# Kernel tuning notes

Hardware: AMD Instinct MI355X
Metric: run time of the kernel (lower is better)

Reference implementation:

```python
import jax, jax.numpy as jnp
import numpy as np

S = 1024      # seq_len
H = 768       # hidden_size
L = 50        # num_labels
E = 65536     # num_edges
SW = 10       # span_width


def setup_inputs() -> dict:
    key = jax.random.key(0)
    ks = jax.random.split(key, 10)
    hidden_states = jax.random.normal(ks[0], (1, S, H), jnp.float32)
    src = jax.random.randint(ks[1], (E,), 0, S)
    tgt = jax.random.randint(ks[2], (E,), 0, S)
    lbl = jax.random.randint(ks[3], (E,), 0, L)
    edges = jnp.stack([src, tgt, lbl], axis=-1)[None].astype(jnp.int32)  # [1,E,3]
    gcn_W = (jax.random.normal(ks[4], (L, H, H)) * 0.02).astype(jnp.float32)
    gcn_b = jnp.zeros((L, H), jnp.float32)
    attn_w = (jax.random.normal(ks[5], (H,)) * 0.02).astype(jnp.float32)
    attn_b = jnp.zeros((), jnp.float32)
    D = 3 * H
    ms_W1 = (jax.random.normal(ks[6], (D, D)) * 0.02).astype(jnp.float32)
    ms_b1 = jnp.zeros((D,), jnp.float32)
    ms_W2 = (jax.random.normal(ks[7], (D,)) * 0.02).astype(jnp.float32)
    ms_b2 = jnp.zeros((), jnp.float32)
    ant_W = (jax.random.normal(ks[8], (2 * D,)) * 0.02).astype(jnp.float32)
    ant_b = jnp.zeros((), jnp.float32)
    # candidate spans exactly as generate_candidate_spans with span_width=SW
    starts, ends = [], []
    for i in range(S):
        for j in range(i + 1, min(i + SW, S)):
            starts.append(i)
            ends.append(j)
    span_starts = jnp.asarray(np.array(starts, dtype=np.int32))
    span_ends = jnp.asarray(np.array(ends, dtype=np.int32))
    topk = int(S * 0.4)  # seq_lens*0.4 with all-ones attention mask
    return {
        'hidden_states': hidden_states, 'edges': edges,
        'gcn_W': gcn_W, 'gcn_b': gcn_b,
        'attn_w': attn_w, 'attn_b': attn_b,
        'ms_W1': ms_W1, 'ms_b1': ms_b1, 'ms_W2': ms_W2, 'ms_b2': ms_b2,
        'ant_W': ant_W, 'ant_b': ant_b,
        'span_starts': span_starts, 'span_ends': span_ends, 'topk': topk,
    }


def reference(hidden_states, edges, gcn_W, gcn_b, attn_w, attn_b,
              ms_W1, ms_b1, ms_W2, ms_b2, ant_W, ant_b,
              span_starts, span_ends, topk):
    B, Sq, Hd = hidden_states.shape  # B == 1
    nl = gcn_W.shape[0]
    x = hidden_states[0]  # [S,H]

    # ---- GCNLayer: per-label linear + scatter-add + degree norm + relu ----
    src = edges[0, :, 0]
    tgt = edges[0, :, 1]
    lbl = edges[0, :, 2]
    # aggregate source embeddings by (target,label): equivalent to applying
    # W_l per edge then index_add, since the transform is linear per label.
    seg = tgt * nl + lbl                               # [E]
    src_emb = x[src]                                   # [E,H]  gather
    agg = jax.ops.segment_sum(src_emb, seg, num_segments=Sq * nl)
    agg = agg.reshape(Sq, nl, Hd)                      # [S,L,H]
    cnt = jax.ops.segment_sum(jnp.ones_like(seg, jnp.float32), seg,
                              num_segments=Sq * nl).reshape(Sq, nl)
    out = jnp.einsum('slh,lhd->sd', agg, gcn_W) + cnt @ gcn_b  # [S,H]
    degree = jnp.clip(cnt.sum(axis=1), 1.0)[:, None]
    gcn_out = jax.nn.relu(out / degree)

    # combine_strategy == 'add'
    emb = x + gcn_out                                  # [S,H]

    # ---- SpanRepresentation: attention pooling over each span ----
    offs = jnp.arange(SW)                              # span length <= SW
    pos = span_starts[:, None] + offs                  # [N,SW]
    valid = pos <= span_ends[:, None]
    pos_c = jnp.minimum(pos, Sq - 1)
    win = emb[pos_c]                                   # [N,SW,H] gather
    scores = win @ attn_w + attn_b                     # [N,SW]
    scores = jnp.where(valid, scores, -1e9)
    aw = jax.nn.softmax(scores, axis=1)
    attn_out = jnp.einsum('nw,nwh->nh', aw, win)       # [N,H]
    span_vec = jnp.concatenate([emb[span_starts], emb[span_ends], attn_out],
                               axis=-1)                # [N,3H]

    # ---- MentionScorer ----
    hdn = jax.nn.relu(span_vec @ ms_W1 + ms_b1)
    mention_scores = hdn @ ms_W2 + ms_b2               # [N]

    # ---- prune_spans: top-k ----
    topk_scores, topk_idx = jax.lax.top_k(mention_scores, topk)
    pruned = span_vec[topk_idx]                        # [k,3H]

    # ---- antecedent scores: linear over concat pair == sum of two matvecs ----
    D = span_vec.shape[-1]
    s_i = pruned @ ant_W[:D]                           # [k]
    s_j = pruned @ ant_W[D:]                           # [k]
    ant_scores = s_i[:, None] + s_j[None, :] + ant_b   # [k,k]
    # triu mask (antecedent must strictly precede the mention)
    k = pruned.shape[0]
    triu = jnp.triu(jnp.ones((k, k), bool), k=0)
    ant_scores = jnp.where(triu, -1e4, ant_scores)
    dummy = jnp.zeros((k, 1), ant_scores.dtype)
    ant_scores_with_dummy = jnp.concatenate([dummy, ant_scores], axis=1)  # [k,k+1]
    return ant_scores_with_dummy
```

## Files before the change

kernel.cpp:

```cpp
#include <hip/hip_runtime.h>
#include <stdint.h>

typedef __attribute__((ext_vector_type(4))) float f32x4;
typedef __attribute__((ext_vector_type(4))) int i32x4;
typedef __attribute__((ext_vector_type(8))) int i32x8;

#define S_TOK 1024
#define H_DIM 768
#define NLBL  50
#define NEDGE 65536
#define NSEG  (S_TOK * NLBL)
#define NSPAN 9171
#define MPAD  9216
#define DDIM  2304
#define KTOP  409

__device__ __forceinline__ unsigned short f32_to_bf16u(float f) {
  unsigned u = __float_as_uint(f);
  u += 0x7fffu + ((u >> 16) & 1u);
  return (unsigned short)(u >> 16);
}
__device__ __forceinline__ float bf16u_to_f32(unsigned short h) {
  return __uint_as_float(((unsigned)h) << 16);
}
__device__ __forceinline__ unsigned short pack_fp8x2(float a, float b) {
  return (unsigned short)(__builtin_amdgcn_cvt_pk_fp8_f32(a, b, 0, false) & 0xffff);
}
__device__ __forceinline__ unsigned pack_fp8x4(float a, float b, float c, float d) {
  int v = __builtin_amdgcn_cvt_pk_fp8_f32(a, b, 0, false);
  v = __builtin_amdgcn_cvt_pk_fp8_f32(c, d, v, true);
  return (unsigned)v;
}
__device__ __forceinline__ unsigned char pack_fp8x1(float a) {
  return (unsigned char)(__builtin_amdgcn_cvt_pk_fp8_f32(a, a, 0, false) & 0xff);
}

__device__ __forceinline__ void gl_lds16(const void* g, void* l) {
  __builtin_amdgcn_global_load_lds((const __attribute__((address_space(1))) void*)g,
                                   (__attribute__((address_space(3))) void*)l, 16, 0, 0);
}

__global__ __launch_bounds__(256) void convert_fp8(
    const float* __restrict__ in, unsigned* __restrict__ out, int nquads) {
  int i = blockIdx.x * 256 + threadIdx.x;
  if (i >= nquads) return;
  float4 v = ((const float4*)in)[i];
  out[i] = pack_fp8x4(v.x, v.y, v.z, v.w);
}

__global__ __launch_bounds__(256) void transpose_fp8_b(
    const float* __restrict__ in, unsigned char* __restrict__ out, int R, int C) {
  __shared__ float tile[32][33];
  size_t boff = (size_t)blockIdx.z * R * C;
  int tx = threadIdx.x & 31, ty = threadIdx.x >> 5;
  int c0 = blockIdx.x * 32, r0 = blockIdx.y * 32;
#pragma unroll
  for (int i = 0; i < 4; i++)
    tile[ty + 8 * i][tx] = in[boff + (size_t)(r0 + ty + 8 * i) * C + c0 + tx];
  __syncthreads();
#pragma unroll
  for (int i = 0; i < 4; i++)
    out[boff + (size_t)(c0 + ty + 8 * i) * R + r0 + tx] = pack_fp8x1(tile[tx][ty + 8 * i]);
}

__global__ void edge_count2(const int* __restrict__ edges, int* __restrict__ seg_count,
                            int* __restrict__ tgt_count) {
  int e = blockIdx.x * 256 + threadIdx.x;
  if (e >= NEDGE) return;
  int tgt = edges[e * 3 + 1], lbl = edges[e * 3 + 2];
  atomicAdd(&seg_count[tgt * NLBL + lbl], 1);
  atomicAdd(&tgt_count[tgt], 1);
}

__global__ __launch_bounds__(1024) void scan_t(
    const int* __restrict__ cnt, int* __restrict__ offs) {
  __shared__ int part[1024];
  int t = threadIdx.x;
  int c = cnt[t];
  part[t] = c;
  __syncthreads();
  for (int o = 1; o < 1024; o <<= 1) {
    int v = part[t];
    int u = (t >= o) ? part[t - o] : 0;
    __syncthreads();
    part[t] = v + u;
    __syncthreads();
  }
  offs[t] = part[t] - c;
  if (t == 1023) offs[1024] = part[t];
}

__global__ void edge_scatter_t(const int* __restrict__ edges, const int* __restrict__ tgt_off,
                               int* __restrict__ cursor, int* __restrict__ sorted_row) {
  int e = blockIdx.x * 256 + threadIdx.x;
  if (e >= NEDGE) return;
  int src = edges[e * 3], tgt = edges[e * 3 + 1], lbl = edges[e * 3 + 2];
  int pos = tgt_off[tgt] + atomicAdd(&cursor[tgt], 1);
  sorted_row[pos] = lbl * S_TOK + src;
}

template <int EPI>
__global__ __launch_bounds__(256) void gemm_fp8(
    const unsigned char* __restrict__ A, const unsigned char* __restrict__ B,
    unsigned char* __restrict__ Y, float* __restrict__ C,
    const float* __restrict__ b1, const float* __restrict__ w2,
    int M, int Nn, int Kb, int mb, size_t strideB, size_t strideY) {
  __shared__ unsigned char As[128 * 128];
  __shared__ unsigned char Bs[128 * 128];
  int im = blockIdx.x % mb, in_ = blockIdx.x / mb;
  int m0 = im * 128, n0 = in_ * 128;
  const unsigned char* Bl = B + (size_t)blockIdx.y * strideB;

  int t = threadIdx.x;
  int wave = t >> 6, lane = t & 63;
  int wr = wave >> 1, wc = wave & 1;
  int quad = lane >> 4, l15 = lane & 15;
  int lrow = lane >> 3;
  int lk = ((lane & 7) ^ lrow) << 4;

  f32x4 acc[4][4];
  f32x4 zero = {0.f, 0.f, 0.f, 0.f};
#pragma unroll
  for (int mi = 0; mi < 4; mi++)
#pragma unroll
    for (int ni = 0; ni < 4; ni++) acc[mi][ni] = zero;

  for (int kt = 0; kt < Kb; kt += 128) {
#pragma unroll
    for (int i = 0; i < 4; i++) {
      int c = i * 4 + wave;
      int r = c * 8 + lrow;
      gl_lds16(A + (size_t)(m0 + r) * Kb + kt + lk, &As[c * 1024]);
      gl_lds16(Bl + (size_t)(n0 + r) * Kb + kt + lk, &Bs[c * 1024]);
    }
    __syncthreads();
    i32x8 af[4], bg[4];
#pragma unroll
    for (int mi = 0; mi < 4; mi++) {
      int r = wr * 64 + mi * 16 + l15;
      int base = r * 128;
      i32x4 lo = *(const i32x4*)&As[base + (((2 * quad) ^ (r & 7)) << 4)];
      i32x4 hi = *(const i32x4*)&As[base + (((2 * quad + 1) ^ (r & 7)) << 4)];
      af[mi] = __builtin_shufflevector(lo, hi, 0, 1, 2, 3, 4, 5, 6, 7);
    }
#pragma unroll
    for (int ni = 0; ni < 4; ni++) {
      int r = wc * 64 + ni * 16 + l15;
      int base = r * 128;
      i32x4 lo = *(const i32x4*)&Bs[base + (((2 * quad) ^ (r & 7)) << 4)];
      i32x4 hi = *(const i32x4*)&Bs[base + (((2 * quad + 1) ^ (r & 7)) << 4)];
      bg[ni] = __builtin_shufflevector(lo, hi, 0, 1, 2, 3, 4, 5, 6, 7);
    }
#pragma unroll
    for (int mi = 0; mi < 4; mi++)
#pragma unroll
      for (int ni = 0; ni < 4; ni++)
        acc[mi][ni] = __builtin_amdgcn_mfma_scale_f32_16x16x128_f8f6f4(
            af[mi], bg[ni], acc[mi][ni], 0, 0, 0, 0x7f7f7f7f, 0, 0x7f7f7f7f);
    __syncthreads();
  }

  if (EPI == 0) {
    unsigned char* Yl = Y + (size_t)blockIdx.y * strideY;
#pragma unroll
    for (int mi = 0; mi < 4; mi++)
#pragma unroll
      for (int ni = 0; ni < 4; ni++)
#pragma unroll
        for (int r = 0; r < 4; r++)
          As[(wr * 64 + mi * 16 + quad * 4 + r) * 128 + wc * 64 + ni * 16 + l15] =
              pack_fp8x1(acc[mi][ni][r]);
    __syncthreads();
#pragma unroll
    for (int i = 0; i < 4; i++) {
      int idx = t + i * 256;
      int row = idx >> 3, off2 = (idx & 7) << 4;
      *(i32x4*)(Yl + (size_t)(m0 + row) * Nn + n0 + off2) = *(const i32x4*)&As[row * 128 + off2];
    }
  } else {
    float b1v[4], w2v[4];
#pragma unroll
    for (int ni = 0; ni < 4; ni++) {
      int gn = n0 + wc * 64 + ni * 16 + l15;
      b1v[ni] = b1[gn];
      w2v[ni] = w2[gn];
    }
#pragma unroll
    for (int mi = 0; mi < 4; mi++) {
      int gm = m0 + wr * 64 + mi * 16 + quad * 4;
      float part[4] = {0.f, 0.f, 0.f, 0.f};
#pragma unroll
      for (int ni = 0; ni < 4; ni++)
#pragma unroll
        for (int r = 0; r < 4; r++)
          part[r] += fmaxf(acc[mi][ni][r] + b1v[ni], 0.f) * w2v[ni];
#pragma unroll
      for (int o = 1; o < 16; o <<= 1)
#pragma unroll
        for (int r = 0; r < 4; r++) part[r] += __shfl_xor(part[r], o, 64);
      if (l15 == 0) {
#pragma unroll
        for (int r = 0; r < 4; r++)
          if (gm + r < M) atomicAdd(&C[gm + r], part[r]);
      }
    }
  }
}

__global__ __launch_bounds__(192) void gather_emb_kernel(
    const float* __restrict__ x, const unsigned char* __restrict__ Y,
    const int* __restrict__ tgt_off, const int* __restrict__ sorted_row,
    const int* __restrict__ seg_count, const float* __restrict__ gcn_b,
    float* __restrict__ emb) {
  int s = blockIdx.x;
  int t = threadIdx.x;
  int b = tgt_off[s], e = tgt_off[s + 1];
  float a0 = 0.f, a1 = 0.f, a2 = 0.f, a3 = 0.f;
  int p = b;
  for (; p + 1 < e; p += 2) {
    const unsigned* r0 = (const unsigned*)(Y + (size_t)sorted_row[p] * H_DIM);
    const unsigned* r1 = (const unsigned*)(Y + (size_t)sorted_row[p + 1] * H_DIM);
    unsigned w0 = r0[t], w1 = r1[t];
    a0 += __builtin_amdgcn_cvt_f32_fp8(w0, 0) + __builtin_amdgcn_cvt_f32_fp8(w1, 0);
    a1 += __builtin_amdgcn_cvt_f32_fp8(w0, 1) + __builtin_amdgcn_cvt_f32_fp8(w1, 1);
    a2 += __builtin_amdgcn_cvt_f32_fp8(w0, 2) + __builtin_amdgcn_cvt_f32_fp8(w1, 2);
    a3 += __builtin_amdgcn_cvt_f32_fp8(w0, 3) + __builtin_amdgcn_cvt_f32_fp8(w1, 3);
  }
  if (p < e) {
    unsigned w0 = ((const unsigned*)(Y + (size_t)sorted_row[p] * H_DIM))[t];
    a0 += __builtin_amdgcn_cvt_f32_fp8(w0, 0);
    a1 += __builtin_amdgcn_cvt_f32_fp8(w0, 1);
    a2 += __builtin_amdgcn_cvt_f32_fp8(w0, 2);
    a3 += __builtin_amdgcn_cvt_f32_fp8(w0, 3);
  }
  float deg = 0.f, b0 = 0.f, b1 = 0.f, b2 = 0.f, b3 = 0.f;
#pragma unroll 5
  for (int l = 0; l < NLBL; l++) {
    float c = (float)seg_count[s * NLBL + l];
    deg += c;
    float4 g = ((const float4*)(gcn_b + l * H_DIM))[t];
    b0 += c * g.x; b1 += c * g.y; b2 += c * g.z; b3 += c * g.w;
  }
  float dinv = 1.f / fmaxf(deg, 1.f);
  float4 xe = ((const float4*)(x + (size_t)s * H_DIM))[t];
  float4 o;
  o.x = xe.x + fmaxf((a0 + b0) * dinv, 0.f);
  o.y = xe.y + fmaxf((a1 + b1) * dinv, 0.f);
  o.z = xe.z + fmaxf((a2 + b2) * dinv, 0.f);
  o.w = xe.w + fmaxf((a3 + b3) * dinv, 0.f);
  ((float4*)(emb + (size_t)s * H_DIM))[t] = o;
}

__global__ __launch_bounds__(256) void span_kernel(
    const float* __restrict__ emb, const float* __restrict__ attn_w,
    unsigned char* __restrict__ spanv) {
  int i = blockIdx.x;
  int nsp = 1023 - i; if (nsp > 9) nsp = 9;
  if (nsp <= 0) return;
  int nrow = nsp + 1;
  __shared__ float rows[10][768];
  __shared__ float dsh[10];
  int t = threadIdx.x;
  for (int idx = t; idx < nrow * 384; idx += 256) {
    int r = idx / 384, c2 = idx % 384;
    float2 v = ((const float2*)(emb + (size_t)(i + r) * H_DIM))[c2];
    rows[r][c2 * 2] = v.x; rows[r][c2 * 2 + 1] = v.y;
  }
  __syncthreads();
  int wave = t >> 6, lane = t & 63;
  for (int w = wave; w < nrow; w += 4) {
    float p = 0.f;
#pragma unroll
    for (int q = 0; q < 12; q++) p += rows[w][lane + 64 * q] * attn_w[lane + 64 * q];
#pragma unroll
    for (int o = 1; o < 64; o <<= 1) p += __shfl_xor(p, o, 64);
    if (lane == 0) dsh[w] = p;
  }
  __syncthreads();
  float d[10], ex[10];
  float mx = -1e30f;
  for (int w = 0; w < nrow; w++) { d[w] = dsh[w]; mx = fmaxf(mx, d[w]); }
  for (int w = 0; w < nrow; w++) ex[w] = __expf(d[w] - mx);
  bool has2 = (t < 128);
  float n00 = ex[0] * rows[0][2 * t], n01 = ex[0] * rows[0][2 * t + 1];
  float n10 = 0.f, n11 = 0.f;
  if (has2) { n10 = ex[0] * rows[0][2 * t + 512]; n11 = ex[0] * rows[0][2 * t + 513]; }
  float S = ex[0];
  int dd = i - 1014;
  int base = 9 * i - (dd > 0 ? dd * (dd - 1) / 2 : 0);
  unsigned short s0a = pack_fp8x2(rows[0][2 * t], rows[0][2 * t + 1]);
  unsigned short s0b = has2 ? pack_fp8x2(rows[0][2 * t + 512], rows[0][2 * t + 513]) : (unsigned short)0;
  for (int k = 1; k <= nsp; k++) {
    S += ex[k];
    n00 += ex[k] * rows[k][2 * t]; n01 += ex[k] * rows[k][2 * t + 1];
    if (has2) { n10 += ex[k] * rows[k][2 * t + 512]; n11 += ex[k] * rows[k][2 * t + 513]; }
    float inv = 1.f / S;
    unsigned short* out16 = (unsigned short*)(spanv + (size_t)(base + k - 1) * DDIM);
    out16[t] = s0a;
    out16[384 + t] = pack_fp8x2(rows[k][2 * t], rows[k][2 * t + 1]);
    out16[768 + t] = pack_fp8x2(n00 * inv, n01 * inv);
    if (has2) {
      out16[t + 256] = s0b;
      out16[384 + t + 256] = pack_fp8x2(rows[k][2 * t + 512], rows[k][2 * t + 513]);
      out16[768 + t + 256] = pack_fp8x2(n10 * inv, n11 * inv);
    }
  }
}

__device__ __forceinline__ unsigned score_key(float s) {
  unsigned b = __float_as_uint(s);
  return (b & 0x80000000u) ? ~b : (b | 0x80000000u);
}

__global__ __launch_bounds__(1024) void topk_kernel(
    const float* __restrict__ scores, int* __restrict__ topk_idx) {
  __shared__ unsigned skeys[NSPAN];
  __shared__ int hist[16 * 256];
  __shared__ int hsum[256];
  __shared__ unsigned sh_prefix;
  __shared__ int sh_remaining, sh_cnt;
  __shared__ unsigned long long keys[512];
  int t = threadIdx.x;
  int wv = t >> 6;
  for (int i = t; i < NSPAN; i += 1024) skeys[i] = score_key(scores[i]);
  unsigned prefix = 0;
  int remaining = KTOP;
  for (int p = 3; p >= 0; p--) {
    for (int b = t; b < 16 * 256; b += 1024) hist[b] = 0;
    __syncthreads();
    for (int i = t; i < NSPAN; i += 1024) {
      unsigned u = skeys[i];
      bool ok = (p == 3) ? true : ((u >> ((p + 1) * 8)) == prefix);
      if (ok) atomicAdd(&hist[wv * 256 + ((u >> (p * 8)) & 0xff)], 1);
    }
    __syncthreads();
    if (t < 256) {
      int s = 0;
#pragma unroll
      for (int w = 0; w < 16; w++) s += hist[w * 256 + t];
      hsum[t] = s;
    }
    __syncthreads();
    if (t == 0) {
      int rem = remaining;
      int b = 255;
      for (;; b--) {
        int c = hsum[b];
        if (c >= rem) break;
        rem -= c;
      }
      sh_prefix = (prefix << 8) | (unsigned)b;
      sh_remaining = rem;
    }
    __syncthreads();
    prefix = sh_prefix;
    remaining = sh_remaining;
    __syncthreads();
  }
  unsigned kth = prefix;
  if (t == 0) sh_cnt = 0;
  __syncthreads();
  for (int i = t; i < NSPAN; i += 1024) {
    unsigned u = skeys[i];
    if (u >= kth) {
      int pos = atomicAdd(&sh_cnt, 1);
      if (pos < 512) keys[pos] = (((unsigned long long)(~u)) << 32) | (unsigned)i;
    }
  }
  __syncthreads();
  int cnt = sh_cnt < 512 ? sh_cnt : 512;
  for (int i = t; i < 512; i += 1024)
    if (i >= cnt) keys[i] = ~0ull;
  __syncthreads();
  for (int ksz = 2; ksz <= 512; ksz <<= 1)
    for (int j = ksz >> 1; j > 0; j >>= 1) {
      if (t < 512) {
        int ixj = t ^ j;
        if (ixj > t) {
          unsigned long long a = keys[t], b = keys[ixj];
          bool up = ((t & ksz) == 0);
          if (up ? (a > b) : (a < b)) { keys[t] = b; keys[ixj] = a; }
        }
      }
      __syncthreads();
    }
  for (int i = t; i < KTOP; i += 1024) topk_idx[i] = (int)(keys[i] & 0xffffffffu);
}

__global__ __launch_bounds__(256) void sij_kernel(
    const unsigned char* __restrict__ spanv, const int* __restrict__ topk_idx,
    const float* __restrict__ antW, float* __restrict__ s_i, float* __restrict__ s_j) {
  int r = blockIdx.x;
  int idx = topk_idx[r];
  const unsigned* row32 = (const unsigned*)(spanv + (size_t)idx * DDIM);
  int t = threadIdx.x, lane = t & 63, wave = t >> 6;
  float pi = 0.f, pj = 0.f;
  for (int q = t; q < DDIM / 4; q += 256) {
    unsigned w = row32[q];
    float v0 = __builtin_amdgcn_cvt_f32_fp8(w, 0);
    float v1 = __builtin_amdgcn_cvt_f32_fp8(w, 1);
    float v2 = __builtin_amdgcn_cvt_f32_fp8(w, 2);
    float v3 = __builtin_amdgcn_cvt_f32_fp8(w, 3);
    const float* ai = antW + q * 4;
    const float* aj = antW + DDIM + q * 4;
    pi += v0 * ai[0] + v1 * ai[1] + v2 * ai[2] + v3 * ai[3];
    pj += v0 * aj[0] + v1 * aj[1] + v2 * aj[2] + v3 * aj[3];
  }
  for (int o = 32; o; o >>= 1) {
    pi += __shfl_down(pi, o, 64);
    pj += __shfl_down(pj, o, 64);
  }
  __shared__ float ri[4], rj[4];
  if (lane == 0) { ri[wave] = pi; rj[wave] = pj; }
  __syncthreads();
  if (t == 0) {
    s_i[r] = ri[0] + ri[1] + ri[2] + ri[3];
    s_j[r] = rj[0] + rj[1] + rj[2] + rj[3];
  }
}

__global__ void out_kernel(const float* __restrict__ s_i, const float* __restrict__ s_j,
                           const float* __restrict__ ant_b, float* __restrict__ out) {
  int idx = blockIdx.x * 256 + threadIdx.x;
  if (idx >= KTOP * (KTOP + 1)) return;
  int i = idx / (KTOP + 1), c = idx % (KTOP + 1);
  float v;
  if (c == 0) v = 0.f;
  else {
    int j = c - 1;
    v = (j >= i) ? -10000.f : (s_i[i] + s_j[j] + ant_b[0]);
  }
  out[idx] = v;
}

extern "C" void kernel_launch(void* const* d_in, const int* in_sizes, int n_in,
                              void* d_out, int out_size, void* d_ws, size_t ws_size,
                              hipStream_t stream) {
  const float* x      = (const float*)d_in[0];
  const int*   edges  = (const int*)d_in[1];
  const float* gcn_W  = (const float*)d_in[2];
  const float* gcn_b  = (const float*)d_in[3];
  const float* attn_w = (const float*)d_in[4];
  const float* ms_W1  = (const float*)d_in[6];
  const float* ms_b1  = (const float*)d_in[7];
  const float* ms_W2  = (const float*)d_in[8];
  const float* ant_W  = (const float*)d_in[10];
  const float* ant_b  = (const float*)d_in[11];

  size_t off = 0;
  char* wsb = (char*)d_ws;
  auto alloc = [&](size_t bytes) -> void* {
    void* p = wsb + off;
    off += (bytes + 255) & ~(size_t)255;
    return p;
  };
  unsigned char* Y     = (unsigned char*)alloc((size_t)NLBL * S_TOK * H_DIM);
  unsigned char* WtB   = (unsigned char*)alloc((size_t)NLBL * H_DIM * H_DIM);
  unsigned char* Wt2   = (unsigned char*)alloc((size_t)DDIM * DDIM);
  unsigned char* spanv = (unsigned char*)alloc((size_t)MPAD * DDIM);
  unsigned char* Xb    = (unsigned char*)alloc((size_t)S_TOK * H_DIM);
  int* seg_count  = (int*)alloc(NSEG * 4);
  int* tgt_count  = (int*)alloc(S_TOK * 4);
  int* cursor     = (int*)alloc(S_TOK * 4);
  float* scores   = (float*)alloc(MPAD * 4);
  size_t zero_bytes = (char*)(scores + MPAD) - (char*)seg_count;
  int* tgt_off    = (int*)alloc((S_TOK + 4) * 4);
  int* sorted_row = (int*)alloc(NEDGE * 4);
  float* emb    = (float*)alloc((size_t)S_TOK * H_DIM * 4);
  int* topk_idx = (int*)alloc(512 * 4);
  float* s_i    = (float*)alloc(512 * 4);
  float* s_j    = (float*)alloc(512 * 4);
  (void)ws_size; (void)in_sizes; (void)n_in; (void)out_size;

  hipMemsetAsync(seg_count, 0, zero_bytes, stream);

  dim3 b256(256);
  convert_fp8<<<(S_TOK * H_DIM / 4 + 255) / 256, b256, 0, stream>>>(x, (unsigned*)Xb,
                                                                    S_TOK * H_DIM / 4);
  transpose_fp8_b<<<dim3(H_DIM / 32, H_DIM / 32, NLBL), b256, 0, stream>>>(gcn_W, WtB, H_DIM, H_DIM);
  transpose_fp8_b<<<dim3(DDIM / 32, DDIM / 32, 1), b256, 0, stream>>>(ms_W1, Wt2, DDIM, DDIM);
  edge_count2<<<NEDGE / 256, b256, 0, stream>>>(edges, seg_count, tgt_count);
  scan_t<<<1, 1024, 0, stream>>>(tgt_count, tgt_off);
  edge_scatter_t<<<NEDGE / 256, b256, 0, stream>>>(edges, tgt_off, cursor, sorted_row);
  gemm_fp8<0><<<dim3(48, NLBL), b256, 0, stream>>>(
      Xb, WtB, Y, nullptr, nullptr, nullptr,
      S_TOK, H_DIM, H_DIM, 8, (size_t)H_DIM * H_DIM, (size_t)S_TOK * H_DIM);
  gather_emb_kernel<<<S_TOK, dim3(192), 0, stream>>>(x, Y, tgt_off, sorted_row, seg_count, gcn_b, emb);
  span_kernel<<<S_TOK, b256, 0, stream>>>(emb, attn_w, spanv);
  gemm_fp8<1><<<dim3(72 * 18, 1), b256, 0, stream>>>(
      spanv, Wt2, nullptr, scores, ms_b1, ms_W2,
      NSPAN, DDIM, DDIM, 72, 0, 0);
  topk_kernel<<<1, 1024, 0, stream>>>(scores, topk_idx);
  sij_kernel<<<KTOP, b256, 0, stream>>>(spanv, topk_idx, ant_W, s_i, s_j);
  out_kernel<<<(KTOP * (KTOP + 1) + 255) / 256, b256, 0, stream>>>(s_i, s_j, ant_b, (float*)d_out);
}
```

Measured before the change: 451.5 us.

## Factor mention-scorer GEMM into per-token projections plus attention-part GEMM

The span vector's first two thirds are just emb[start] and emb[end], so their contribution to span_vec @ W1 is precomputed once per token as a 1024x4608 projection P. The big 9216x2304x2304 GEMM shrinks to K=768 over the attention part, with P gathered in the epilogue by start/end index. spanv storage is replaced by a compact attention-only buffer plus packed start/end indices, and sij reads the sections separately. This cuts mention-scorer FLOPs and span writes roughly threefold. The cost is an extra GEMM, a new fp8 conversion of emb, and scattered fp32 reads of P in the epilogue.

```diff
diff --git a/kernel.cpp b/kernel.cpp
--- a/kernel.cpp
+++ b/kernel.cpp
@@ -14,6 +14,7 @@
 #define MPAD  9216
 #define DDIM  2304
 #define KTOP  409
+#define PSTRIDE 4608
 
 __device__ __forceinline__ unsigned short f32_to_bf16u(float f) {
   unsigned u = __float_as_uint(f);
@@ -61,6 +62,25 @@
 #pragma unroll
   for (int i = 0; i < 4; i++)
     out[boff + (size_t)(c0 + ty + 8 * i) * R + r0 + tx] = pack_fp8x1(tile[tx][ty + 8 * i]);
+}
+
+__global__ __launch_bounds__(256) void transpose_fp8_p(
+    const float* __restrict__ in, unsigned char* __restrict__ out) {
+  __shared__ float tile[32][33];
+  int tx = threadIdx.x & 31, ty = threadIdx.x >> 5;
+  int c0 = blockIdx.x * 32;
+  int r0 = blockIdx.y * 32;
+#pragma unroll
+  for (int i = 0; i < 4; i++)
+    tile[ty + 8 * i][tx] = in[(size_t)(r0 + ty + 8 * i) * DDIM + c0 + tx];
+  __syncthreads();
+  int half = (r0 >= 768) ? 1 : 0;
+  int hbase = r0 - half * 768;
+#pragma unroll
+  for (int i = 0; i < 4; i++) {
+    int d = c0 + ty + 8 * i, h = hbase + tx;
+    out[(size_t)(d + half * DDIM) * H_DIM + h] = pack_fp8x1(tile[tx][ty + 8 * i]);
+  }
 }
 
 __global__ void edge_count2(const int* __restrict__ edges, int* __restrict__ seg_count,
@@ -104,6 +124,7 @@
     const unsigned char* __restrict__ A, const unsigned char* __restrict__ B,
     unsigned char* __restrict__ Y, float* __restrict__ C,
     const float* __restrict__ b1, const float* __restrict__ w2,
+    const float* __restrict__ P, const int* __restrict__ se,
     int M, int Nn, int Kb, int mb, size_t strideB, size_t strideY) {
   __shared__ unsigned char As[128 * 128];
   __shared__ unsigned char Bs[128 * 128];
@@ -177,23 +198,33 @@
       int row = idx >> 3, off2 = (idx & 7) << 4;
       *(i32x4*)(Yl + (size_t)(m0 + row) * Nn + n0 + off2) = *(const i32x4*)&As[row * 128 + off2];
     }
-  } else {
+  } else if (EPI == 1) {
     float b1v[4], w2v[4];
+    int gnb = n0 + wc * 64 + l15;
 #pragma unroll
     for (int ni = 0; ni < 4; ni++) {
-      int gn = n0 + wc * 64 + ni * 16 + l15;
+      int gn = gnb + ni * 16;
       b1v[ni] = b1[gn];
       w2v[ni] = w2[gn];
     }
 #pragma unroll
     for (int mi = 0; mi < 4; mi++) {
       int gm = m0 + wr * 64 + mi * 16 + quad * 4;
-      float part[4] = {0.f, 0.f, 0.f, 0.f};
-#pragma unroll
-      for (int ni = 0; ni < 4; ni++)
-#pragma unroll
-        for (int r = 0; r < 4; r++)
-          part[r] += fmaxf(acc[mi][ni][r] + b1v[ni], 0.f) * w2v[ni];
+      float part[4];
+#pragma unroll
+      for (int r = 0; r < 4; r++) {
+        int sev = se[gm + r];
+        const float* Ps = P + (size_t)(sev >> 10) * PSTRIDE;
+        const float* Pe = P + (size_t)(sev & 1023) * PSTRIDE + DDIM;
+        float pr = 0.f;
+#pragma unroll
+        for (int ni = 0; ni < 4; ni++) {
+          int gn = gnb + ni * 16;
+          float v = acc[mi][ni][r] + Ps[gn] + Pe[gn] + b1v[ni];
+          pr += fmaxf(v, 0.f) * w2v[ni];
+        }
+        part[r] = pr;
+      }
 #pragma unroll
       for (int o = 1; o < 16; o <<= 1)
 #pragma unroll
@@ -202,6 +233,18 @@
 #pragma unroll
         for (int r = 0; r < 4; r++)
           if (gm + r < M) atomicAdd(&C[gm + r], part[r]);
+      }
+    }
+  } else {
+#pragma unroll
+    for (int mi = 0; mi < 4; mi++) {
+      int gm = m0 + wr * 64 + mi * 16 + quad * 4;
+#pragma unroll
+      for (int ni = 0; ni < 4; ni++) {
+        int gn = n0 + wc * 64 + ni * 16 + l15;
+#pragma unroll
+        for (int r = 0; r < 4; r++)
+          C[(size_t)(gm + r) * Nn + gn] = acc[mi][ni][r];
       }
     }
   }
@@ -253,7 +296,7 @@
 
 __global__ __launch_bounds__(256) void span_kernel(
     const float* __restrict__ emb, const float* __restrict__ attn_w,
-    unsigned char* __restrict__ spanv) {
+    unsigned char* __restrict__ spanvA, int* __restrict__ se) {
   int i = blockIdx.x;
   int nsp = 1023 - i; if (nsp > 9) nsp = 9;
   if (nsp <= 0) return;
@@ -288,22 +331,16 @@
   float S = ex[0];
   int dd = i - 1014;
   int base = 9 * i - (dd > 0 ? dd * (dd - 1) / 2 : 0);
-  unsigned short s0a = pack_fp8x2(rows[0][2 * t], rows[0][2 * t + 1]);
-  unsigned short s0b = has2 ? pack_fp8x2(rows[0][2 * t + 512], rows[0][2 * t + 513]) : (unsigned short)0;
   for (int k = 1; k <= nsp; k++) {
     S += ex[k];
     n00 += ex[k] * rows[k][2 * t]; n01 += ex[k] * rows[k][2 * t + 1];
     if (has2) { n10 += ex[k] * rows[k][2 * t + 512]; n11 += ex[k] * rows[k][2 * t + 513]; }
     float inv = 1.f / S;
-    unsigned short* out16 = (unsigned short*)(spanv + (size_t)(base + k - 1) * DDIM);
-    out16[t] = s0a;
-    out16[384 + t] = pack_fp8x2(rows[k][2 * t], rows[k][2 * t + 1]);
-    out16[768 + t] = pack_fp8x2(n00 * inv, n01 * inv);
-    if (has2) {
-      out16[t + 256] = s0b;
-      out16[384 + t + 256] = pack_fp8x2(rows[k][2 * t + 512], rows[k][2 * t + 513]);
-      out16[768 + t + 256] = pack_fp8x2(n10 * inv, n11 * inv);
-    }
+    int m = base + k - 1;
+    unsigned short* out16 = (unsigned short*)(spanvA + (size_t)m * H_DIM);
+    out16[t] = pack_fp8x2(n00 * inv, n01 * inv);
+    if (has2) out16[256 + t] = pack_fp8x2(n10 * inv, n11 * inv);
+    if (t == 0) se[m] = (i << 10) | (i + k);
   }
 }
 
@@ -388,15 +425,21 @@
 }
 
 __global__ __launch_bounds__(256) void sij_kernel(
-    const unsigned char* __restrict__ spanv, const int* __restrict__ topk_idx,
+    const unsigned char* __restrict__ embf8, const unsigned char* __restrict__ spanvA,
+    const int* __restrict__ se, const int* __restrict__ topk_idx,
     const float* __restrict__ antW, float* __restrict__ s_i, float* __restrict__ s_j) {
   int r = blockIdx.x;
   int idx = topk_idx[r];
-  const unsigned* row32 = (const unsigned*)(spanv + (size_t)idx * DDIM);
+  int sev = se[idx];
+  const unsigned* sec0 = (const unsigned*)(embf8 + (size_t)(sev >> 10) * H_DIM);
+  const unsigned* sec1 = (const unsigned*)(embf8 + (size_t)(sev & 1023) * H_DIM);
+  const unsigned* sec2 = (const unsigned*)(spanvA + (size_t)idx * H_DIM);
   int t = threadIdx.x, lane = t & 63, wave = t >> 6;
   float pi = 0.f, pj = 0.f;
   for (int q = t; q < DDIM / 4; q += 256) {
-    unsigned w = row32[q];
+    int sec = q / 192, w32 = q - sec * 192;
+    const unsigned* p32 = (sec == 0) ? sec0 : (sec == 1) ? sec1 : sec2;
+    unsigned w = p32[w32];
     float v0 = __builtin_amdgcn_cvt_f32_fp8(w, 0);
     float v1 = __builtin_amdgcn_cvt_f32_fp8(w, 1);
     float v2 = __builtin_amdgcn_cvt_f32_fp8(w, 2);
@@ -456,14 +499,18 @@
   };
   unsigned char* Y     = (unsigned char*)alloc((size_t)NLBL * S_TOK * H_DIM);
   unsigned char* WtB   = (unsigned char*)alloc((size_t)NLBL * H_DIM * H_DIM);
-  unsigned char* Wt2   = (unsigned char*)alloc((size_t)DDIM * DDIM);
-  unsigned char* spanv = (unsigned char*)alloc((size_t)MPAD * DDIM);
+  unsigned char* WtP   = (unsigned char*)alloc((size_t)2 * DDIM * H_DIM);
+  unsigned char* WtC   = (unsigned char*)alloc((size_t)DDIM * H_DIM);
+  unsigned char* spanvA = (unsigned char*)alloc((size_t)MPAD * H_DIM);
   unsigned char* Xb    = (unsigned char*)alloc((size_t)S_TOK * H_DIM);
+  unsigned char* Embf8 = (unsigned char*)alloc((size_t)S_TOK * H_DIM);
+  float* P             = (float*)alloc((size_t)S_TOK * PSTRIDE * 4);
   int* seg_count  = (int*)alloc(NSEG * 4);
   int* tgt_count  = (int*)alloc(S_TOK * 4);
   int* cursor     = (int*)alloc(S_TOK * 4);
   float* scores   = (float*)alloc(MPAD * 4);
-  size_t zero_bytes = (char*)(scores + MPAD) - (char*)seg_count;
+  int* se         = (int*)alloc(MPAD * 4);
+  size_t zero_bytes = (char*)(se + MPAD) - (char*)seg_count;
   int* tgt_off    = (int*)alloc((S_TOK + 4) * 4);
   int* sorted_row = (int*)alloc(NEDGE * 4);
   float* emb    = (float*)alloc((size_t)S_TOK * H_DIM * 4);
@@ -478,19 +525,26 @@
   convert_fp8<<<(S_TOK * H_DIM / 4 + 255) / 256, b256, 0, stream>>>(x, (unsigned*)Xb,
                                                                     S_TOK * H_DIM / 4);
   transpose_fp8_b<<<dim3(H_DIM / 32, H_DIM / 32, NLBL), b256, 0, stream>>>(gcn_W, WtB, H_DIM, H_DIM);
-  transpose_fp8_b<<<dim3(DDIM / 32, DDIM / 32, 1), b256, 0, stream>>>(ms_W1, Wt2, DDIM, DDIM);
+  transpose_fp8_p<<<dim3(DDIM / 32, 1536 / 32), b256, 0, stream>>>(ms_W1, WtP);
+  transpose_fp8_b<<<dim3(DDIM / 32, H_DIM / 32, 1), b256, 0, stream>>>(
+      ms_W1 + (size_t)1536 * DDIM, WtC, H_DIM, DDIM);
   edge_count2<<<NEDGE / 256, b256, 0, stream>>>(edges, seg_count, tgt_count);
   scan_t<<<1, 1024, 0, stream>>>(tgt_count, tgt_off);
   edge_scatter_t<<<NEDGE / 256, b256, 0, stream>>>(edges, tgt_off, cursor, sorted_row);
   gemm_fp8<0><<<dim3(48, NLBL), b256, 0, stream>>>(
-      Xb, WtB, Y, nullptr, nullptr, nullptr,
+      Xb, WtB, Y, nullptr, nullptr, nullptr, nullptr, nullptr,
       S_TOK, H_DIM, H_DIM, 8, (size_t)H_DIM * H_DIM, (size_t)S_TOK * H_DIM);
   gather_emb_kernel<<<S_TOK, dim3(192), 0, stream>>>(x, Y, tgt_off, sorted_row, seg_count, gcn_b, emb);
-  span_kernel<<<S_TOK, b256, 0, stream>>>(emb, attn_w, spanv);
+  convert_fp8<<<(S_TOK * H_DIM / 4 + 255) / 256, b256, 0, stream>>>(emb, (unsigned*)Embf8,
+                                                                    S_TOK * H_DIM / 4);
+  gemm_fp8<2><<<dim3(8 * 36, 1), b256, 0, stream>>>(
+      Embf8, WtP, nullptr, P, nullptr, nullptr, nullptr, nullptr,
+      S_TOK, PSTRIDE, H_DIM, 8, 0, 0);
+  span_kernel<<<S_TOK, b256, 0, stream>>>(emb, attn_w, spanvA, se);
   gemm_fp8<1><<<dim3(72 * 18, 1), b256, 0, stream>>>(
-      spanv, Wt2, nullptr, scores, ms_b1, ms_W2,
-      NSPAN, DDIM, DDIM, 72, 0, 0);
+      spanvA, WtC, nullptr, scores, ms_b1, ms_W2, P, se,
+      NSPAN, DDIM, H_DIM, 72, 0, 0);
   topk_kernel<<<1, 1024, 0, stream>>>(scores, topk_idx);
-  sij_kernel<<<KTOP, b256, 0, stream>>>(spanv, topk_idx, ant_W, s_i, s_j);
+  sij_kernel<<<KTOP, b256, 0, stream>>>(Embf8, spanvA, se, topk_idx, ant_W, s_i, s_j);
   out_kernel<<<(KTOP * (KTOP + 1) + 255) / 256, b256, 0, stream>>>(s_i, s_j, ant_b, (float*)d_out);
 }
```

After: 454.6 us. No clear change (+0.7%).
